# Optimization experiments

Measured on AMD Instinct MI355X. Metric: run time of the kernel, lower is better.

Reference implementation:

```python
import jax, jax.numpy as jnp
import numpy as np

B, T, D, H, K = 2, 1024, 1024, 16, 64
DMIX, DDEC, DA = 32, 64, 64
EPS = 1e-5 * 64  # GroupNorm eps = 1e-5 * head_size_divisor**2


def setup_inputs() -> dict:
    keys = jax.random.split(jax.random.key(0), 12)
    r01 = 12.0 / 23.0   # layer_id / (num_hidden_layers - 1)
    r1a0 = 0.5          # 1 - layer_id / num_hidden_layers
    ddd = np.arange(D, dtype=np.float32) / D
    maa = lambda p: jnp.asarray((1.0 - ddd ** p).reshape(1, 1, D), jnp.float32)
    decay = -6.0 + 5.0 * (np.arange(D, dtype=np.float32) / (D - 1)) ** (0.7 + 1.3 * r01)
    u = lambda i, s: jax.random.uniform(keys[i], s, jnp.float32, -0.01, 0.01)
    lin = lambda i: jax.random.normal(keys[i], (D, D), jnp.float32) / np.sqrt(D)
    return dict(
        x=jax.random.normal(keys[0], (B, T, D), jnp.float32),
        time_maa_x=maa(r1a0), time_maa_w=maa(r1a0), time_maa_k=maa(r1a0),
        time_maa_v=jnp.asarray((1.0 - (ddd ** r1a0 + 0.3 * r01)).reshape(1, 1, D), jnp.float32),
        time_maa_r=maa(0.5 * r1a0), time_maa_g=maa(0.5 * r1a0), time_maa_a=maa(r1a0),
        time_maa_w1=u(1, (D, DMIX * 6)), time_maa_w2=u(2, (6, DMIX, D)),
        time_decay=jnp.asarray(decay.reshape(1, 1, D), jnp.float32),
        time_decay_w1=u(3, (D, DDEC)), time_decay_w2=u(4, (DDEC, D)),
        a0=jnp.zeros((1, 1, D), jnp.float32),
        a1=u(5, (D, DA)) * 10.0,
        a2=jax.random.normal(keys[6], (DA, D), jnp.float32) * 0.1,
        k_k=jnp.full((1, 1, D), 0.85, jnp.float32),
        k_a=jnp.ones((1, 1, D), jnp.float32),
        W_r=lin(7), W_k=lin(8), W_v=lin(9), W_g=lin(10), W_o=lin(11),
        ln_w=jnp.ones((D,), jnp.float32), ln_b=jnp.zeros((D,), jnp.float32),
    )


def reference(x, time_maa_x, time_maa_w, time_maa_k, time_maa_v, time_maa_r,
              time_maa_g, time_maa_a, time_maa_w1, time_maa_w2, time_decay,
              time_decay_w1, time_decay_w2, a0, a1, a2, k_k, k_a,
              W_r, W_k, W_v, W_g, W_o, ln_w, ln_b):
    Bx, Tx, Dx = x.shape
    # bidirectional token shift: mean of left/right neighbors
    left = jnp.pad(x[:, :-1], ((0, 0), (1, 0), (0, 0)))
    right = jnp.pad(x[:, 1:], ((0, 0), (0, 1), (0, 0)))
    dxprev = (left + right) * 0.5 - x

    # data-dependent mixing coefficients (6-way LoRA)
    xxx = x + dxprev * time_maa_x
    hmix = jnp.tanh(xxx @ time_maa_w1).reshape(Bx, Tx, 6, DMIX)
    mix = jnp.einsum('btsm,smd->sbtd', hmix, time_maa_w2)  # (6,B,T,D)
    mw, mk, mv, mr, mg, ma = mix
    xw = x + dxprev * (time_maa_w + mw)
    xk = x + dxprev * (time_maa_k + mk)
    xv = x + dxprev * (time_maa_v + mv)
    xr = x + dxprev * (time_maa_r + mr)
    xg = x + dxprev * (time_maa_g + mg)
    xa = x + dxprev * (time_maa_a + ma)

    r = xr @ W_r
    k = xk @ W_k
    v = xv @ W_v
    g = jax.nn.silu(xg @ W_g)
    w = time_decay + jnp.tanh(xw @ time_decay_w1) @ time_decay_w2
    iclr = jax.nn.sigmoid(a0 + (xa @ a1) @ a2)
    kkh = (k * k_k).reshape(Bx, Tx, H, K)
    kk = kkh / jnp.maximum(jnp.linalg.norm(kkh, axis=-1, keepdims=True), 1e-12)
    kk = kk.reshape(Bx, Tx, Dx)
    k = k * (1.0 + (iclr - 1.0) * k_a)

    heads = lambda t: t.reshape(Bx, Tx, H, K).transpose(0, 2, 1, 3)  # (B,H,T,K)
    r_h, k_h, v_h, kk_h, iclr_h = map(heads, (r, k, v, kk, iclr))
    w_h = -jnp.exp(heads(w))

    # LION bidirectional attention with delta correction (quadratic form)
    cs = jnp.cumsum(w_h, axis=2)
    cs_b = cs - w_h
    cs_f = jnp.clip(cs - cs[:, :, Tx // 2:Tx // 2 + 1, :], -60.0, 60.0)
    cs_bs = jnp.clip(cs_b - cs_b[:, :, Tx // 2:Tx // 2 + 1, :], -60.0, 60.0)
    A_fwd = jnp.tril(jnp.einsum('bhik,bhjk->bhij', r_h * jnp.exp(cs_f), k_h * jnp.exp(-cs_f)))
    A_bwd = jnp.triu(jnp.einsum('bhik,bhjk->bhij', r_h * jnp.exp(-cs_bs), k_h * jnp.exp(cs_bs)), k=1)
    kk_corr = jnp.einsum('bhik,bhjk->bhij', kk_h * iclr_h, kk_h)
    A_df = -jnp.tril(A_fwd @ jnp.tril(kk_corr, -1))
    A_db = -jnp.triu(A_bwd @ jnp.triu(kk_corr, 1), k=1)
    y = (A_fwd + A_bwd + A_df + A_db) @ v_h  # (B,H,T,K)

    # GroupNorm(n_head groups) over flattened tokens
    y = y.transpose(0, 2, 1, 3).reshape(Bx * Tx, H, K)
    mu = y.mean(axis=-1, keepdims=True)
    var = y.var(axis=-1, keepdims=True)
    y = (y - mu) / jnp.sqrt(var + EPS)
    y = y.reshape(Bx, Tx, Dx) * ln_w + ln_b
    return (y * g) @ W_o
```

## Files before the change

### kernel.cpp

```cpp
#include <hip/hip_runtime.h>
#include <math.h>

#define BB 2
#define TT 1024
#define DD 1024
#define HH 16
#define KK 64
#define NBT 2048
#define NE  2097152ULL

typedef unsigned short u16;
typedef __attribute__((ext_vector_type(8))) short short8;
typedef __attribute__((ext_vector_type(4))) short short4v;
typedef __attribute__((ext_vector_type(4))) float f32x4;

__device__ __forceinline__ float bf2f(u16 u) {
  union { unsigned int i; float f; } v; v.i = ((unsigned int)u) << 16; return v.f;
}
__device__ __forceinline__ u16 f2bf(float x) {
  union { float f; unsigned int u; } v; v.f = x;
  unsigned int r = v.u + 0x7fffu + ((v.u >> 16) & 1u);
  return (u16)(r >> 16);
}
__device__ __forceinline__ f32x4 MFMA(short8 a, short8 b, f32x4 c) {
  return __builtin_amdgcn_mfma_f32_16x16x32_bf16(a, b, c, 0, 0, 0);
}
__device__ __forceinline__ int swzb(int row, int kbyte) {
  return row * 128 + (kbyte ^ ((row & 7) << 4));
}
__device__ __forceinline__ void gload16(const void* g, void* l) {
  __builtin_amdgcn_global_load_lds((const __attribute__((address_space(1))) void*)g,
                                   (__attribute__((address_space(3))) void*)l, 16, 0, 0);
}

__global__ __launch_bounds__(256)
void pre(const float* __restrict__ W2, u16* __restrict__ W2t,
         const float* __restrict__ W1, u16* __restrict__ W1t,
         const float* __restrict__ wdec2, const float* __restrict__ a2,
         u16* __restrict__ wdec2t, u16* __restrict__ a2t,
         const float* __restrict__ wdec1, const float* __restrict__ a1,
         u16* __restrict__ wdec1t, u16* __restrict__ a1t,
         const float* __restrict__ x, const float* __restrict__ maa_x,
         u16* __restrict__ xxx_b) {
  __shared__ float tl[64][65];
  int idx = blockIdx.x;
  int tid = threadIdx.x;
  if (idx < 96) {
    int s = idx >> 4, d0 = (idx & 15) * 64;
    int c = tid & 63, r0 = (tid >> 6) * 8;
#pragma unroll
    for (int j = 0; j < 8; ++j)
      tl[r0 + j][c] = W2[(size_t)(s * 32 + r0 + j) * 1024 + d0 + c];
    __syncthreads();
    int d = tid >> 2, ms = (tid & 3) * 8;
    u16 o[8];
#pragma unroll
    for (int j = 0; j < 8; ++j) o[j] = f2bf(tl[ms + j][d]);
    *(short8*)(W2t + ((size_t)s * 1024 + d0 + d) * 32 + ms) = *(short8*)o;
  } else if (idx < 144) {
    int i = idx - 96;
    int k0 = (i & 15) * 64, n0 = (i >> 4) * 64;
    int r = tid >> 2, c0 = (tid & 3) * 16;
#pragma unroll
    for (int j = 0; j < 16; j += 4) {
      f32x4 v = *(const f32x4*)(W1 + (size_t)(k0 + r) * 192 + n0 + c0 + j);
      tl[r][c0 + j + 0] = v[0]; tl[r][c0 + j + 1] = v[1];
      tl[r][c0 + j + 2] = v[2]; tl[r][c0 + j + 3] = v[3];
    }
    __syncthreads();
    u16 o[16];
#pragma unroll
    for (int j = 0; j < 16; ++j) o[j] = f2bf(tl[c0 + j][r]);
    *(short8*)(W1t + (size_t)(n0 + r) * 1024 + k0 + c0) = *(short8*)(o);
    *(short8*)(W1t + (size_t)(n0 + r) * 1024 + k0 + c0 + 8) = *(short8*)(o + 8);
  } else if (idx < 176) {
    int i = idx - 144;
    int zz = i >> 4;
    const float* W = zz ? a2 : wdec2;
    u16* Wt = zz ? a2t : wdec2t;
    int n0 = (i & 15) * 64;
    int r = tid >> 2, c0 = (tid & 3) * 16;
#pragma unroll
    for (int j = 0; j < 16; j += 4) {
      f32x4 v = *(const f32x4*)(W + (size_t)r * 1024 + n0 + c0 + j);
      tl[r][c0 + j + 0] = v[0]; tl[r][c0 + j + 1] = v[1];
      tl[r][c0 + j + 2] = v[2]; tl[r][c0 + j + 3] = v[3];
    }
    __syncthreads();
    u16 o[16];
#pragma unroll
    for (int j = 0; j < 16; ++j) o[j] = f2bf(tl[c0 + j][r]);
    *(short8*)(Wt + (size_t)(n0 + r) * 64 + c0) = *(short8*)(o);
    *(short8*)(Wt + (size_t)(n0 + r) * 64 + c0 + 8) = *(short8*)(o + 8);
  } else if (idx < 208) {
    int i = idx - 176;
    int zz = i >> 4;
    const float* W = zz ? a1 : wdec1;
    u16* Wt = zz ? a1t : wdec1t;
    int k0 = (i & 15) * 64;
    int r = tid >> 2, c0 = (tid & 3) * 16;
#pragma unroll
    for (int j = 0; j < 16; j += 4) {
      f32x4 v = *(const f32x4*)(W + (size_t)(k0 + r) * 64 + c0 + j);
      tl[r][c0 + j + 0] = v[0]; tl[r][c0 + j + 1] = v[1];
      tl[r][c0 + j + 2] = v[2]; tl[r][c0 + j + 3] = v[3];
    }
    __syncthreads();
    u16 o[16];
#pragma unroll
    for (int j = 0; j < 16; ++j) o[j] = f2bf(tl[c0 + j][r]);
    *(short8*)(Wt + (size_t)r * 1024 + k0 + c0) = *(short8*)(o);
    *(short8*)(Wt + (size_t)r * 1024 + k0 + c0 + 8) = *(short8*)(o + 8);
  } else {
    int row = idx - 208;
    int t = row & (TT - 1);
    int d0 = tid * 4;
    size_t g = (size_t)row * DD + d0;
    f32x4 xc = *(const f32x4*)(x + g);
    f32x4 xl = {0.f, 0.f, 0.f, 0.f}, xr = {0.f, 0.f, 0.f, 0.f};
    if (t != 0) xl = *(const f32x4*)(x + g - DD);
    if (t != TT - 1) xr = *(const f32x4*)(x + g + DD);
    f32x4 mx = *(const f32x4*)(maa_x + d0);
    u16 o[4];
#pragma unroll
    for (int j = 0; j < 4; ++j)
      o[j] = f2bf(xc[j] + (0.5f * (xl[j] + xr[j]) - xc[j]) * mx[j]);
    *(short4v*)(xxx_b + g) = *(short4v*)o;
  }
}

__global__ __launch_bounds__(256)
void hmix_g(const float* __restrict__ W_r, const float* __restrict__ W_k,
            const float* __restrict__ W_v, const float* __restrict__ W_g,
            const float* __restrict__ W_o,
            u16* __restrict__ TR, u16* __restrict__ TK, u16* __restrict__ TV,
            u16* __restrict__ TG, u16* __restrict__ TO,
            const u16* __restrict__ xxx_b, const u16* __restrict__ W1t,
            float* __restrict__ P3) {
  __shared__ float tl[64][65];
  __shared__ u16 As[4096];
  __shared__ u16 Bs[2048];
  int idx = blockIdx.x;
  int tid = threadIdx.x;
  if (idx < 1280) {
    int z = idx >> 8, rem = idx & 255;
    const float* W = (z == 0) ? W_r : (z == 1) ? W_k : (z == 2) ? W_v : (z == 3) ? W_g : W_o;
    u16* Wt = (z == 0) ? TR : (z == 1) ? TK : (z == 2) ? TV : (z == 3) ? TG : TO;
    int k0 = (rem & 15) * 64, n0 = (rem >> 4) * 64;
    int r = tid >> 2, c0 = (tid & 3) * 16;
#pragma unroll
    for (int j = 0; j < 16; j += 4) {
      f32x4 v = *(const f32x4*)(W + (size_t)(k0 + r) * 1024 + n0 + c0 + j);
      tl[r][c0 + j + 0] = v[0]; tl[r][c0 + j + 1] = v[1];
      tl[r][c0 + j + 2] = v[2]; tl[r][c0 + j + 3] = v[3];
    }
    __syncthreads();
    u16 o[16];
#pragma unroll
    for (int j = 0; j < 16; ++j) o[j] = f2bf(tl[c0 + j][r]);
    *(short8*)(Wt + (size_t)(n0 + r) * 1024 + k0 + c0) = *(short8*)(o);
    *(short8*)(Wt + (size_t)(n0 + r) * 1024 + k0 + c0 + 8) = *(short8*)(o + 8);
    return;
  }
  int i = idx - 1280;
  int n0 = (i % 3) * 64;
  int q = i / 3;
  int m0 = (q & 15) * 128;
  int kb = q >> 4;
  int w = tid >> 6, lane = tid & 63;
  int mq = w >> 1, nq = w & 1;
  f32x4 acc[4][2];
#pragma unroll
  for (int ii = 0; ii < 4; ++ii)
#pragma unroll
    for (int j = 0; j < 2; ++j) acc[ii][j] = {0.f, 0.f, 0.f, 0.f};
  for (int t = 0; t < 4; ++t) {
    int k0 = kb * 128 + t * 32;
#pragma unroll
    for (int c2 = 0; c2 < 2; ++c2) {
      int ch = w * 2 + c2;
      int row = ch * 16 + (lane >> 2);
      gload16(xxx_b + (size_t)(m0 + row) * 1024 + k0 + (lane & 3) * 8, As + ch * 512);
    }
    {
      int row = w * 16 + (lane >> 2);
      gload16(W1t + (size_t)(n0 + row) * 1024 + k0 + (lane & 3) * 8, Bs + w * 512);
    }
    __syncthreads();
    short8 a[4], b[2];
#pragma unroll
    for (int mf = 0; mf < 4; ++mf)
      a[mf] = *(const short8*)(As + (mq * 64 + mf * 16 + (lane & 15)) * 32 + (lane >> 4) * 8);
#pragma unroll
    for (int nf = 0; nf < 2; ++nf)
      b[nf] = *(const short8*)(Bs + (nq * 32 + nf * 16 + (lane & 15)) * 32 + (lane >> 4) * 8);
#pragma unroll
    for (int mf = 0; mf < 4; ++mf)
#pragma unroll
      for (int nf = 0; nf < 2; ++nf) acc[mf][nf] = MFMA(a[mf], b[nf], acc[mf][nf]);
    __syncthreads();
  }
#pragma unroll
  for (int mf = 0; mf < 4; ++mf) {
#pragma unroll
    for (int nf = 0; nf < 2; ++nf) {
      int mb = m0 + mq * 64 + mf * 16 + (lane >> 4) * 4;
      int n = n0 + nq * 32 + nf * 16 + (lane & 15);
#pragma unroll
      for (int r = 0; r < 4; ++r)
        P3[(size_t)kb * 393216 + (size_t)(mb + r) * 192 + n] = acc[mf][nf][r];
    }
  }
}

__global__ __launch_bounds__(256)
void reduce8b(const float* __restrict__ P, u16* __restrict__ C, int total) {
  size_t i = (size_t)blockIdx.x * 256 + threadIdx.x;
  float s = 0.f;
#pragma unroll
  for (int kb = 0; kb < 8; ++kb) s += P[(size_t)kb * total + i];
  C[i] = f2bf(tanhf(s));
}

__global__ __launch_bounds__(256)
void reduce8_pairb(const float* __restrict__ Pw, const float* __restrict__ Pa,
                   u16* __restrict__ hdec_b, u16* __restrict__ ha_b) {
  int z = blockIdx.y;
  size_t i = (size_t)blockIdx.x * 256 + threadIdx.x;
  const float* P = z ? Pa : Pw;
  float s = 0.f;
#pragma unroll
  for (int kb = 0; kb < 8; ++kb) s += P[(size_t)kb * 131072 + i];
  if (z) ha_b[i] = f2bf(s);
  else hdec_b[i] = f2bf(tanhf(s));
}

__global__ __launch_bounds__(256)
void mixg(const u16* __restrict__ hmixb, const u16* __restrict__ W2t,
          const float* __restrict__ x,
          const float* __restrict__ maa_w, const float* __restrict__ maa_k,
          const float* __restrict__ maa_v, const float* __restrict__ maa_r,
          const float* __restrict__ maa_g, const float* __restrict__ maa_a,
          u16* __restrict__ xw_b, u16* __restrict__ xa_b,
          u16* __restrict__ xk_b, u16* __restrict__ xv_b,
          u16* __restrict__ xr_b, u16* __restrict__ xg_b) {
  __shared__ u16 shm[16384];
  u16* As = shm;
  u16* Bs = shm + 4096;
  u16* mixt = shm;
  int s = blockIdx.z;
  int m0 = blockIdx.y * 128, n0 = blockIdx.x * 128;
  int tid = threadIdx.x, w = tid >> 6, lane = tid & 63;
  int mq = w >> 1, nq = w & 1;
#pragma unroll
  for (int c2 = 0; c2 < 2; ++c2) {
    int ch = w * 2 + c2;
    int row = ch * 16 + (lane >> 2);
    gload16(hmixb + (size_t)(m0 + row) * 192 + s * 32 + (lane & 3) * 8, As + ch * 512);
    gload16(W2t + ((size_t)s * 1024 + n0 + row) * 32 + (lane & 3) * 8, Bs + ch * 512);
  }
  __syncthreads();
  short8 a[4], b[4];
#pragma unroll
  for (int mf = 0; mf < 4; ++mf)
    a[mf] = *(const short8*)(As + (mq * 64 + mf * 16 + (lane & 15)) * 32 + (lane >> 4) * 8);
#pragma unroll
  for (int nf = 0; nf < 4; ++nf)
    b[nf] = *(const short8*)(Bs + (nq * 64 + nf * 16 + (lane & 15)) * 32 + (lane >> 4) * 8);
  f32x4 acc[4][4];
#pragma unroll
  for (int mf = 0; mf < 4; ++mf)
#pragma unroll
    for (int nf = 0; nf < 4; ++nf) {
      f32x4 z = {0.f, 0.f, 0.f, 0.f};
      acc[mf][nf] = MFMA(a[mf], b[nf], z);
    }
  __syncthreads();
#pragma unroll
  for (int mf = 0; mf < 4; ++mf) {
#pragma unroll
    for (int nf = 0; nf < 4; ++nf) {
      int col = nq * 64 + nf * 16 + (lane & 15);
#pragma unroll
      for (int r = 0; r < 4; ++r) {
        int row = mq * 64 + mf * 16 + (lane >> 4) * 4 + r;
        mixt[row * 128 + col] = f2bf(acc[mf][nf][r]);
      }
    }
  }
  __syncthreads();
  const float* maa = (s == 0) ? maa_w : (s == 1) ? maa_k : (s == 2) ? maa_v
                    : (s == 3) ? maa_r : (s == 4) ? maa_g : maa_a;
  u16* dst = (s == 0) ? xw_b : (s == 1) ? xk_b : (s == 2) ? xv_b
            : (s == 3) ? xr_b : (s == 4) ? xg_b : xa_b;
  int cg = tid & 15;
  int rowg = tid >> 4;
  int d0 = n0 + cg * 8;
  f32x4 ma0 = *(const f32x4*)(maa + d0);
  f32x4 ma1 = *(const f32x4*)(maa + d0 + 4);
#pragma unroll
  for (int rr = 0; rr < 8; ++rr) {
    int row = rr * 16 + rowg;
    int m = m0 + row;
    int t = m & (TT - 1);
    size_t g = (size_t)m * DD + d0;
    f32x4 xc0 = *(const f32x4*)(x + g);
    f32x4 xc1 = *(const f32x4*)(x + g + 4);
    f32x4 xl0 = {0.f, 0.f, 0.f, 0.f}, xl1 = {0.f, 0.f, 0.f, 0.f};
    f32x4 xr0 = {0.f, 0.f, 0.f, 0.f}, xr1 = {0.f, 0.f, 0.f, 0.f};
    if (t != 0) { xl0 = *(const f32x4*)(x + g - DD); xl1 = *(const f32x4*)(x + g - DD + 4); }
    if (t != TT - 1) { xr0 = *(const f32x4*)(x + g + DD); xr1 = *(const f32x4*)(x + g + DD + 4); }
    short8 mv = *(const short8*)(mixt + row * 128 + cg * 8);
    u16 o[8];
#pragma unroll
    for (int j = 0; j < 8; ++j) {
      float xcj = (j < 4) ? xc0[j & 3] : xc1[j & 3];
      float xlj = (j < 4) ? xl0[j & 3] : xl1[j & 3];
      float xrj = (j < 4) ? xr0[j & 3] : xr1[j & 3];
      float maj = (j < 4) ? ma0[j & 3] : ma1[j & 3];
      float dx = 0.5f * (xlj + xrj) - xcj;
      o[j] = f2bf(xcj + dx * (maj + bf2f((u16)mv[j])));
    }
    *(short8*)(dst + g) = *(short8*)o;
  }
}

__global__ __launch_bounds__(256)
void gemm_bf4(const u16* __restrict__ xr, const u16* __restrict__ xk,
              const u16* __restrict__ xv, const u16* __restrict__ xg,
              const u16* __restrict__ WtR, const u16* __restrict__ WtK,
              const u16* __restrict__ WtV, const u16* __restrict__ WtG,
              u16* __restrict__ rbuf, u16* __restrict__ kbuf,
              u16* __restrict__ vT, u16* __restrict__ gb,
              const u16* __restrict__ xw_b, const u16* __restrict__ wdec1t,
              float* __restrict__ PpartW,
              const u16* __restrict__ xa_b, const u16* __restrict__ a1t,
              float* __restrict__ PpartA) {
  __shared__ u16 As[2][4096];
  __shared__ u16 Bs[2][2048];
  int wgid = blockIdx.x;
  int tid = threadIdx.x, w = tid >> 6, lane = tid & 63;
  int mq = w >> 1, nq = w & 1;
  if (wgid >= 1024) {
    int i = wgid - 1024;
    int m0 = (i & 15) * 128;
    int kb = (i >> 4) & 7;
    int z = i >> 7;
    const u16* A = z ? xa_b : xw_b;
    const u16* Bt = z ? a1t : wdec1t;
    float* P = z ? PpartA : PpartW;
    f32x4 acc[4][2];
#pragma unroll
    for (int ii = 0; ii < 4; ++ii)
#pragma unroll
      for (int j = 0; j < 2; ++j) acc[ii][j] = {0.f, 0.f, 0.f, 0.f};
    for (int t = 0; t < 4; ++t) {
      int k0 = kb * 128 + t * 32;
#pragma unroll
      for (int c2 = 0; c2 < 2; ++c2) {
        int ch = w * 2 + c2;
        int row = ch * 16 + (lane >> 2);
        gload16(A + (size_t)(m0 + row) * 1024 + k0 + (lane & 3) * 8, As[0] + ch * 512);
      }
      {
        int row = w * 16 + (lane >> 2);
        gload16(Bt + (size_t)row * 1024 + k0 + (lane & 3) * 8, Bs[0] + w * 512);
      }
      __syncthreads();
      short8 a[4], b[2];
#pragma unroll
      for (int mf = 0; mf < 4; ++mf)
        a[mf] = *(const short8*)(As[0] + (mq * 64 + mf * 16 + (lane & 15)) * 32 + (lane >> 4) * 8);
#pragma unroll
      for (int nf = 0; nf < 2; ++nf)
        b[nf] = *(const short8*)(Bs[0] + (nq * 32 + nf * 16 + (lane & 15)) * 32 + (lane >> 4) * 8);
#pragma unroll
      for (int mf = 0; mf < 4; ++mf)
#pragma unroll
        for (int nf = 0; nf < 2; ++nf) acc[mf][nf] = MFMA(a[mf], b[nf], acc[mf][nf]);
      __syncthreads();
    }
#pragma unroll
    for (int mf = 0; mf < 4; ++mf) {
#pragma unroll
      for (int nf = 0; nf < 2; ++nf) {
        int mb = m0 + mq * 64 + mf * 16 + (lane >> 4) * 4;
        int n = nq * 32 + nf * 16 + (lane & 15);
#pragma unroll
        for (int r = 0; r < 4; ++r)
          P[(size_t)kb * 131072 + (size_t)(mb + r) * 64 + n] = acc[mf][nf][r];
      }
    }
    return;
  }
  int xcd = wgid & 7, idx = wgid >> 3;
  int z = xcd >> 1, mhalf = xcd & 1;
  int mloc = idx & 7, nt = idx >> 3;
  int m0 = (mhalf * 8 + mloc) * 128;
  int n0 = nt * 64;
  const u16* A = (z == 0) ? xr : (z == 1) ? xk : (z == 2) ? xv : xg;
  const u16* Bt = (z == 0) ? WtR : (z == 1) ? WtK : (z == 2) ? WtV : WtG;
  int arow0 = (w * 2) * 16 + (lane >> 2);
  int arow1 = (w * 2 + 1) * 16 + (lane >> 2);
  int brow = w * 16 + (lane >> 2);
  int kc = (lane & 3) * 8;
  f32x4 acc[4][2];
#pragma unroll
  for (int i = 0; i < 4; ++i)
#pragma unroll
    for (int j = 0; j < 2; ++j) acc[i][j] = {0.f, 0.f, 0.f, 0.f};
  gload16(A + (size_t)(m0 + arow0) * 1024 + kc, As[0] + (w * 2) * 512);
  gload16(A + (size_t)(m0 + arow1) * 1024 + kc, As[0] + (w * 2 + 1) * 512);
  gload16(Bt + (size_t)(n0 + brow) * 1024 + kc, Bs[0] + w * 512);
  __syncthreads();
  for (int t = 0; t < 32; ++t) {
    int cur = t & 1;
    if (t < 31) {
      int kn = (t + 1) * 32;
      gload16(A + (size_t)(m0 + arow0) * 1024 + kn + kc, As[cur ^ 1] + (w * 2) * 512);
      gload16(A + (size_t)(m0 + arow1) * 1024 + kn + kc, As[cur ^ 1] + (w * 2 + 1) * 512);
      gload16(Bt + (size_t)(n0 + brow) * 1024 + kn + kc, Bs[cur ^ 1] + w * 512);
    }
    short8 a[4], b[2];
#pragma unroll
    for (int mf = 0; mf < 4; ++mf)
      a[mf] = *(const short8*)(As[cur] + (mq * 64 + mf * 16 + (lane & 15)) * 32 + (lane >> 4) * 8);
#pragma unroll
    for (int nf = 0; nf < 2; ++nf)
      b[nf] = *(const short8*)(Bs[cur] + (nq * 32 + nf * 16 + (lane & 15)) * 32 + (lane >> 4) * 8);
#pragma unroll
    for (int mf = 0; mf < 4; ++mf)
#pragma unroll
      for (int nf = 0; nf < 2; ++nf) acc[mf][nf] = MFMA(a[mf], b[nf], acc[mf][nf]);
    __syncthreads();
  }
#pragma unroll
  for (int mf = 0; mf < 4; ++mf) {
#pragma unroll
    for (int nf = 0; nf < 2; ++nf) {
      int mb = m0 + mq * 64 + mf * 16 + (lane >> 4) * 4;
      int n = n0 + nq * 32 + nf * 16 + (lane & 15);
      if (z == 2) {
        u16 o[4];
#pragma unroll
        for (int r = 0; r < 4; ++r) o[r] = f2bf(acc[mf][nf][r]);
        int b2 = mb >> 10, t = mb & 1023;
        *(short4v*)(vT + (((size_t)(b2 * HH + (n >> 6))) * KK + (n & 63)) * TT + t) = *(short4v*)o;
      } else if (z == 3) {
#pragma unroll
        for (int r = 0; r < 4; ++r) {
          int m = mb + r;
          float v = acc[mf][nf][r];
          gb[(size_t)m * 1024 + n] = f2bf(v / (1.f + __expf(-v)));
        }
      } else {
        u16* C = (z == 0) ? rbuf : kbuf;
#pragma unroll
        for (int r = 0; r < 4; ++r) {
          int m = mb + r;
          int b2 = m >> 10, t = m & 1023;
          C[(((size_t)(b2 * HH + (n >> 6))) * TT + t) * KK + (n & 63)] = f2bf(acc[mf][nf][r]);
        }
      }
    }
  }
}

__global__ __launch_bounds__(256)
void gemm_bfo(const u16* __restrict__ A, const u16* __restrict__ Bt,
              float* __restrict__ C) {
  __shared__ u16 As[2][4096];
  __shared__ u16 Bs[2][2048];
  int wgid = blockIdx.x;
  int xcd = wgid & 7, idx = wgid >> 3;
  int mloc = idx & 1, nt = idx >> 1;
  int m0 = (xcd * 2 + mloc) * 128;
  int n0 = nt * 64;
  int tid = threadIdx.x, w = tid >> 6, lane = tid & 63;
  int mq = w >> 1, nq = w & 1;
  int arow0 = (w * 2) * 16 + (lane >> 2);
  int arow1 = (w * 2 + 1) * 16 + (lane >> 2);
  int brow = w * 16 + (lane >> 2);
  int kc = (lane & 3) * 8;
  f32x4 acc[4][2];
#pragma unroll
  for (int i = 0; i < 4; ++i)
#pragma unroll
    for (int j = 0; j < 2; ++j) acc[i][j] = {0.f, 0.f, 0.f, 0.f};
  gload16(A + (size_t)(m0 + arow0) * 1024 + kc, As[0] + (w * 2) * 512);
  gload16(A + (size_t)(m0 + arow1) * 1024 + kc, As[0] + (w * 2 + 1) * 512);
  gload16(Bt + (size_t)(n0 + brow) * 1024 + kc, Bs[0] + w * 512);
  __syncthreads();
  for (int t = 0; t < 32; ++t) {
    int cur = t & 1;
    if (t < 31) {
      int kn = (t + 1) * 32;
      gload16(A + (size_t)(m0 + arow0) * 1024 + kn + kc, As[cur ^ 1] + (w * 2) * 512);
      gload16(A + (size_t)(m0 + arow1) * 1024 + kn + kc, As[cur ^ 1] + (w * 2 + 1) * 512);
      gload16(Bt + (size_t)(n0 + brow) * 1024 + kn + kc, Bs[cur ^ 1] + w * 512);
    }
    short8 a[4], b[2];
#pragma unroll
    for (int mf = 0; mf < 4; ++mf)
      a[mf] = *(const short8*)(As[cur] + (mq * 64 + mf * 16 + (lane & 15)) * 32 + (lane >> 4) * 8);
#pragma unroll
    for (int nf = 0; nf < 2; ++nf)
      b[nf] = *(const short8*)(Bs[cur] + (nq * 32 + nf * 16 + (lane & 15)) * 32 + (lane >> 4) * 8);
#pragma unroll
    for (int mf = 0; mf < 4; ++mf)
#pragma unroll
      for (int nf = 0; nf < 2; ++nf) acc[mf][nf] = MFMA(a[mf], b[nf], acc[mf][nf]);
    __syncthreads();
  }
#pragma unroll
  for (int mf = 0; mf < 4; ++mf) {
#pragma unroll
    for (int nf = 0; nf < 2; ++nf) {
      int mb = m0 + mq * 64 + mf * 16 + (lane >> 4) * 4;
      int n = n0 + nq * 32 + nf * 16 + (lane & 15);
#pragma unroll
      for (int r = 0; r < 4; ++r)
        C[(size_t)(mb + r) * 1024 + n] = acc[mf][nf][r];
    }
  }
}

__global__ __launch_bounds__(256)
void gemm_k2b(const u16* __restrict__ A0, const u16* __restrict__ B0t,
              float* __restrict__ C0, const float* __restrict__ bias0,
              const u16* __restrict__ A1, const u16* __restrict__ B1t,
              float* __restrict__ C1, const float* __restrict__ bias1) {
  __shared__ u16 As[8192];
  __shared__ u16 Bs[4096];
  int z = blockIdx.z;
  const u16* A = z ? A1 : A0;
  const u16* Bt = z ? B1t : B0t;
  float* C = z ? C1 : C0;
  const float* bias = z ? bias1 : bias0;
  int n0 = blockIdx.x * 64, m0 = blockIdx.y * 128;
  int tid = threadIdx.x, w = tid >> 6, lane = tid & 63;
  int mq = w >> 1, nq = w & 1;
#pragma unroll
  for (int j = 0; j < 4; ++j) {
    int q = w * 4 + j;
    int ks = q >> 3, rg = q & 7;
    int row = rg * 16 + (lane >> 2);
    int kc = ks * 32 + (lane & 3) * 8;
    gload16(A + (size_t)(m0 + row) * 64 + kc, As + q * 512);
  }
#pragma unroll
  for (int j = 0; j < 2; ++j) {
    int q = w * 2 + j;
    int ks = q >> 2, rg = q & 3;
    int row = rg * 16 + (lane >> 2);
    int kc = ks * 32 + (lane & 3) * 8;
    gload16(Bt + (size_t)(n0 + row) * 64 + kc, Bs + q * 512);
  }
  __syncthreads();
  f32x4 acc[4][2];
#pragma unroll
  for (int i = 0; i < 4; ++i)
#pragma unroll
    for (int j = 0; j < 2; ++j) acc[i][j] = {0.f, 0.f, 0.f, 0.f};
#pragma unroll
  for (int ks = 0; ks < 2; ++ks) {
    short8 a[4], b[2];
#pragma unroll
    for (int mf = 0; mf < 4; ++mf)
      a[mf] = *(const short8*)(As + ks * 4096 + (mq * 64 + mf * 16 + (lane & 15)) * 32 + (lane >> 4) * 8);
#pragma unroll
    for (int nf = 0; nf < 2; ++nf)
      b[nf] = *(const short8*)(Bs + ks * 2048 + (nq * 32 + nf * 16 + (lane & 15)) * 32 + (lane >> 4) * 8);
#pragma unroll
    for (int mf = 0; mf < 4; ++mf)
#pragma unroll
      for (int nf = 0; nf < 2; ++nf) acc[mf][nf] = MFMA(a[mf], b[nf], acc[mf][nf]);
  }
#pragma unroll
  for (int mf = 0; mf < 4; ++mf) {
#pragma unroll
    for (int nf = 0; nf < 2; ++nf) {
      int mb = m0 + mq * 64 + mf * 16 + (lane >> 4) * 4;
      int n = n0 + nq * 32 + nf * 16 + (lane & 15);
      float bv = bias[n];
#pragma unroll
      for (int r = 0; r < 4; ++r) {
        int m = mb + r;
        int b2 = m >> 10, t = m & 1023;
        float vv = acc[mf][nf][r] + bv;
        if (z) vv = 1.f / (1.f + expf(-vv));
        C[(((size_t)(b2 * HH + (n >> 6))) * TT + t) * KK + (n & 63)] = vv;
      }
    }
  }
}

__global__ __launch_bounds__(256)
void k4k5(u16* __restrict__ kbuf, u16* __restrict__ kkbuf, u16* __restrict__ kkibuf,
          const float* __restrict__ iclr, const float* __restrict__ k_k,
          const float* __restrict__ k_a,
          const float* __restrict__ csf, float* __restrict__ csbs,
          float* __restrict__ part) {
  int idx = blockIdx.x;
  int tid = threadIdx.x;
  if (idx < 8192) {
    int gid = idx * 4 + (tid >> 6);
    int lane = tid & 63;
    size_t base = (size_t)gid * 64 + lane;
    int h = (gid >> 10) & (HH - 1);
    int d = h * 64 + lane;
    float kv = bf2f(kbuf[base]);
    float ic = iclr[base];
    float kkh = kv * k_k[d];
    float ss = kkh * kkh;
#pragma unroll
    for (int off = 32; off > 0; off >>= 1) ss += __shfl_xor(ss, off);
    float nrm = fmaxf(sqrtf(ss), 1e-12f);
    float kkv = kkh / nrm;
    kkbuf[base] = f2bf(kkv);
    kkibuf[base] = f2bf(kkv * ic);
    kbuf[base] = f2bf(kv * (1.f + (ic - 1.f) * k_a[d]));
  } else {
    int bc = (idx - 8192) * 4 + (tid >> 6);
    int bh = bc >> 4, c = bc & 15;
    int lane = tid & 63;
    size_t base = (size_t)bh * TT * KK + (size_t)c * 64 * KK + lane;
    float p = 0.f;
    for (int i = 0; i < 64; ++i) {
      float wh = -expf(csf[base + (size_t)i * KK]);
      csbs[base + (size_t)i * KK] = wh;
      p += wh;
    }
    part[((size_t)bh * 16 + c) * 64 + lane] = p;
  }
}

struct SReg { short8 a0, a1, b0, b1; };
template <int RSA, int RSB>
__device__ __forceinline__ void sload(const u16* ka, const u16* vb, SReg& r) {
  int t0 = threadIdx.x, t1 = threadIdx.x + 256;
  r.a0 = *(const short8*)(ka + (size_t)(t0 >> 3) * RSA + (t0 & 7) * 8);
  r.a1 = *(const short8*)(ka + (size_t)(t1 >> 3) * RSA + (t1 & 7) * 8);
  r.b0 = *(const short8*)(vb + (size_t)(t0 >> 3) * RSB + (t0 & 7) * 8);
  r.b1 = *(const short8*)(vb + (size_t)(t1 >> 3) * RSB + (t1 & 7) * 8);
}
__device__ __forceinline__ void swrite(u16* Kt, u16* Vt, const SReg& r) {
  int t0 = threadIdx.x, t1 = threadIdx.x + 256;
  *(short8*)((char*)Kt + swzb(t0 >> 3, (t0 & 7) * 16)) = r.a0;
  *(short8*)((char*)Kt + swzb(t1 >> 3, (t1 & 7) * 16)) = r.a1;
  *(short8*)((char*)Vt + swzb(t0 >> 3, (t0 & 7) * 16)) = r.b0;
  *(short8*)((char*)Vt + swzb(t1 >> 3, (t1 & 7) * 16)) = r.b1;
}
template <int MASK>
__device__ __forceinline__ void store_S(const f32x4 s[4], u16* St, int lane, int w) {
  int ig0 = w * 16 + (lane >> 4) * 4;
#pragma unroll
  for (int jf = 0; jf < 4; ++jf) {
    int jl = jf * 16 + (lane & 15);
#pragma unroll
    for (int r = 0; r < 4; ++r) {
      int il = ig0 + r;
      float v = s[jf][r];
      if (MASK == 1 && !(jl < il)) v = 0.f;
      if (MASK == 2 && !(jl > il)) v = 0.f;
      if (MASK == 3 && !(jl <= il)) v = 0.f;
      *(u16*)((char*)St + swzb(il, jl * 2)) = f2bf(v);
    }
  }
}
__device__ __forceinline__ void smm(short8 a0, short8 a1, const u16* Kt, f32x4 s[4], int lane) {
  __builtin_amdgcn_s_setprio(1);
#pragma unroll
  for (int jf = 0; jf < 4; ++jf) {
    f32x4 z = {0.f, 0.f, 0.f, 0.f};
    short8 kb0 = *(const short8*)((const char*)Kt + swzb(jf * 16 + (lane & 15), (lane >> 4) * 16));
    z = MFMA(a0, kb0, z);
    short8 kb1 = *(const short8*)((const char*)Kt + swzb(jf * 16 + (lane & 15), 64 + (lane >> 4) * 16));
    z = MFMA(a1, kb1, z);
    s[jf] = z;
  }
  __builtin_amdgcn_s_setprio(0);
}
__device__ __forceinline__ void pv(const u16* St, const u16* Vt, f32x4 acc[4], int lane, int w) {
  __builtin_amdgcn_s_setprio(1);
#pragma unroll
  for (int ks = 0; ks < 2; ++ks) {
    short8 a = *(const short8*)((const char*)St + swzb(w * 16 + (lane & 15), ks * 64 + (lane >> 4) * 16));
#pragma unroll
    for (int cf = 0; cf < 4; ++cf) {
      short8 b = *(const short8*)((const char*)Vt + swzb(cf * 16 + (lane & 15), ks * 64 + (lane >> 4) * 16));
      acc[cf] = MFMA(a, b, acc[cf]);
    }
  }
  __builtin_amdgcn_s_setprio(0);
}

__global__ __launch_bounds__(256)
void k6_pass1(const u16* __restrict__ kk, const u16* __restrict__ kki,
              const u16* __restrict__ vT, u16* __restrict__ vfT, u16* __restrict__ vbT,
              const float* __restrict__ csbs, const float* __restrict__ part,
              const u16* __restrict__ rb, const u16* __restrict__ kb,
              u16* __restrict__ rfb, u16* __restrict__ rbb,
              u16* __restrict__ kfb, u16* __restrict__ kbw) {
  __shared__ u16 Kt[2][4096], Vt[2][4096], St[4096];
  int wg = blockIdx.x;
  int tid = threadIdx.x;
  if (wg >= 1024) {
    int bc = (wg - 1024) * 4 + (tid >> 6);
    int bh = bc >> 4, c = bc & 15;
    int lane = tid & 63;
    size_t hb = (size_t)bh * TT * KK;
    float run = 0.f, csb512 = 0.f;
    for (int cc = 0; cc < 16; ++cc) {
      float pvv = part[((size_t)bh * 16 + cc) * 64 + lane];
      if (cc < c) run += pvv;
      if (cc < 8) csb512 += pvv;
    }
    float wh512 = csbs[hb + (size_t)512 * KK + lane];
    float cs512 = csb512 + wh512;
    size_t base = hb + (size_t)c * 64 * KK + lane;
    float cs = run;
    for (int i = 0; i < 64; ++i) {
      size_t g = base + (size_t)i * KK;
      float wh = csbs[g];
      cs += wh;
      float cf = fminf(fmaxf(cs - cs512, -60.f), 60.f);
      float cb = fminf(fmaxf((cs - wh) - csb512, -60.f), 60.f);
      float rvf = bf2f(rb[g]);
      float kvf = bf2f(kb[g]);
      rfb[g] = f2bf(rvf * __expf(cf));
      kfb[g] = f2bf(kvf * __expf(-cf));
      rbb[g] = f2bf(rvf * __expf(-cb));
      kbw[g] = f2bf(kvf * __expf(cb));
    }
    return;
  }
  int dir = (wg >= 512);
  int w0 = dir ? wg - 512 : wg;
  int bh = w0 & 31, it = w0 >> 5, i0 = it * 64;
  size_t hb = (size_t)bh * 65536;
  int w = tid >> 6, lane = tid & 63;
  int iw = i0 + w * 16;
  int row = iw + (lane & 15), ko = (lane >> 4) * 8;
  short8 a0 = *(const short8*)(kki + hb + (size_t)row * 64 + ko);
  short8 a1 = *(const short8*)(kki + hb + (size_t)row * 64 + 32 + ko);
  f32x4 acc[4];
#pragma unroll
  for (int c = 0; c < 4; ++c) acc[c] = {0.f, 0.f, 0.f, 0.f};
  int s0 = dir ? it : 0;
  int nph = dir ? 16 - it : it + 1;
  SReg sr, nx;
  sload<64, 1024>(kk + hb + (size_t)s0 * 4096, vT + hb + s0 * 64, sr);
  swrite(Kt[0], Vt[0], sr);
  __syncthreads();
  for (int p = 0; p < nph; ++p) {
    int s = s0 + p;
    int cur = p & 1;
    if (p < nph - 1)
      sload<64, 1024>(kk + hb + (size_t)(s + 1) * 4096, vT + hb + (s + 1) * 64, nx);
    f32x4 sv[4];
    smm(a0, a1, Kt[cur], sv, lane);
    if (s == it) {
      if (dir) store_S<2>(sv, St, lane, w);
      else store_S<1>(sv, St, lane, w);
    } else {
      store_S<0>(sv, St, lane, w);
    }
    pv(St, Vt[cur], acc, lane, w);
    if (p < nph - 1) swrite(Kt[cur ^ 1], Vt[cur ^ 1], nx);
    __syncthreads();
  }
  u16* dst = dir ? vbT : vfT;
#pragma unroll
  for (int cf = 0; cf < 4; ++cf) {
    int c = cf * 16 + (lane & 15);
    int i = iw + (lane >> 4) * 4;
    size_t g = hb + (size_t)c * 1024 + i;
    short4v vv = *(const short4v*)(vT + g);
    u16 o1[4];
#pragma unroll
    for (int r = 0; r < 4; ++r)
      o1[r] = f2bf(bf2f((u16)vv[r]) - acc[cf][r]);
    *(short4v*)(dst + g) = *(short4v*)o1;
  }
}

__global__ __launch_bounds__(256)
void k7_pass2(const u16* __restrict__ rfb, const u16* __restrict__ rbb,
              const u16* __restrict__ kfb, const u16* __restrict__ kbw,
              const u16* __restrict__ vfT, const u16* __restrict__ vbT,
              float* __restrict__ yf, float* __restrict__ yb) {
  __shared__ u16 Kt[2][4096], Vt[2][4096], St[4096];
  int wg = blockIdx.x;
  int dir = (wg >= 512);
  int w0 = dir ? wg - 512 : wg;
  int bh = w0 & 31, it = w0 >> 5, i0 = it * 64;
  size_t hb = (size_t)bh * 65536;
  int tid = threadIdx.x, w = tid >> 6, lane = tid & 63;
  int iw = i0 + w * 16;
  int row = iw + (lane & 15), ko = (lane >> 4) * 8;
  const u16* rp = dir ? rbb : rfb;
  const u16* kp = dir ? kbw : kfb;
  const u16* vp = dir ? vbT : vfT;
  short8 a0 = *(const short8*)(rp + hb + (size_t)row * 64 + ko);
  short8 a1 = *(const short8*)(rp + hb + (size_t)row * 64 + 32 + ko);
  f32x4 acc[4];
#pragma unroll
  for (int c = 0; c < 4; ++c) acc[c] = {0.f, 0.f, 0.f, 0.f};
  int s0 = dir ? it : 0;
  int nph = dir ? 16 - it : it + 1;
  SReg sr, nx;
  sload<64, 1024>(kp + hb + (size_t)s0 * 4096, vp + hb + s0 * 64, sr);
  swrite(Kt[0], Vt[0], sr);
  __syncthreads();
  for (int p = 0; p < nph; ++p) {
    int s = s0 + p;
    int cur = p & 1;
    if (p < nph - 1)
      sload<64, 1024>(kp + hb + (size_t)(s + 1) * 4096, vp + hb + (s + 1) * 64, nx);
    f32x4 sv[4];
    smm(a0, a1, Kt[cur], sv, lane);
    if (s == it) {
      if (dir) store_S<2>(sv, St, lane, w);
      else store_S<3>(sv, St, lane, w);
    } else {
      store_S<0>(sv, St, lane, w);
    }
    pv(St, Vt[cur], acc, lane, w);
    if (p < nph - 1) swrite(Kt[cur ^ 1], Vt[cur ^ 1], nx);
    __syncthreads();
  }
  float* y = dir ? yb : yf;
#pragma unroll
  for (int cf = 0; cf < 4; ++cf) {
    int c = cf * 16 + (lane & 15);
#pragma unroll
    for (int r = 0; r < 4; ++r) {
      int i = iw + (lane >> 4) * 4 + r;
      y[hb + (size_t)i * 64 + c] = acc[cf][r];
    }
  }
}

__global__ __launch_bounds__(256)
void k8_gn2(const float* __restrict__ yf, const float* __restrict__ yb,
            const u16* __restrict__ g, const float* __restrict__ lnw,
            const float* __restrict__ lnb, u16* __restrict__ outb) {
  int bt = blockIdx.x;
  int b = bt >> 10, t = bt & 1023;
  int wv = threadIdx.x >> 6, lane = threadIdx.x & 63;
  for (int h = wv; h < HH; h += 4) {
    size_t idx = (((size_t)(b * HH + h)) * TT + t) * KK + lane;
    float v = yf[idx] + yb[idx];
    float s1 = v, s2 = v * v;
#pragma unroll
    for (int off = 32; off > 0; off >>= 1) {
      s1 += __shfl_xor(s1, off);
      s2 += __shfl_xor(s2, off);
    }
    float mu = s1 * (1.f / 64.f);
    float var = s2 * (1.f / 64.f) - mu * mu;
    float xn = (v - mu) * rsqrtf(var + 6.4e-4f);
    int d = h * 64 + lane;
    float o = xn * lnw[d] + lnb[d];
    outb[(size_t)bt * DD + d] = f2bf(o * bf2f(g[(size_t)bt * DD + d]));
  }
}

extern "C" void kernel_launch(void* const* d_in, const int* in_sizes, int n_in,
                              void* d_out, int out_size, void* d_ws, size_t ws_size,
                              hipStream_t stream) {
  const float* x      = (const float*)d_in[0];
  const float* maa_x  = (const float*)d_in[1];
  const float* maa_w  = (const float*)d_in[2];
  const float* maa_k  = (const float*)d_in[3];
  const float* maa_v  = (const float*)d_in[4];
  const float* maa_r  = (const float*)d_in[5];
  const float* maa_g  = (const float*)d_in[6];
  const float* maa_a  = (const float*)d_in[7];
  const float* w1mix  = (const float*)d_in[8];
  const float* w2mix  = (const float*)d_in[9];
  const float* tdecay = (const float*)d_in[10];
  const float* wdec1  = (const float*)d_in[11];
  const float* wdec2  = (const float*)d_in[12];
  const float* a0     = (const float*)d_in[13];
  const float* a1     = (const float*)d_in[14];
  const float* a2     = (const float*)d_in[15];
  const float* k_k    = (const float*)d_in[16];
  const float* k_a    = (const float*)d_in[17];
  const float* W_r    = (const float*)d_in[18];
  const float* W_k    = (const float*)d_in[19];
  const float* W_v    = (const float*)d_in[20];
  const float* W_g    = (const float*)d_in[21];
  const float* W_o    = (const float*)d_in[22];
  const float* lnw    = (const float*)d_in[23];
  const float* lnb    = (const float*)d_in[24];
  float* out = (float*)d_out;

  const size_t NEf = NE;
  float* F = (float*)d_ws;
  u16*   xxx_b  = (u16*)F;
  u16*   xw_b   = (u16*)(F + 1 * NEf);
  u16*   xa_b   = (u16*)(F + 2 * NEf);
  float* csfb   = F + 3 * NEf;
  float* csbsb  = F + 4 * NEf;
  float* P3     = F + 3 * NEf;
  float* PpartW = F + 3 * NEf;
  float* PpartA = F + 4 * NEf;
  float* yf     = F + 3 * NEf;
  float* yb     = F + 4 * NEf;
  float* iclr   = F + 5 * NEf;
  u16*   gb     = (u16*)(F + 6 * NEf);
  u16*   hmixb  = (u16*)(F + 7 * NEf);
  u16*   hdec_b = (u16*)(F + 7 * NEf + 524288);
  u16*   ha_b   = (u16*)(F + 7 * NEf + 786432);
  float* partb  = F + 7 * NEf + 917504;
  u16*   W1t    = (u16*)(F + 7 * NEf + 1048576);
  u16*   wdec2t = (u16*)(F + 7 * NEf + 1146880);
  u16*   a2t    = (u16*)(F + 7 * NEf + 1179648);
  u16*   wdec1t = (u16*)(F + 7 * NEf + 1212416);
  u16*   a1t    = (u16*)(F + 7 * NEf + 1245184);
  u16*   W2t    = (u16*)(F + 7 * NEf + 1966080);
  u16* rfb = (u16*)xw_b;
  u16* rbb = rfb + NEf;
  u16* kfb = (u16*)xa_b;
  u16* kbw = kfb + NEf;
  u16* U = (u16*)(F + 8 * NEf);
  u16* xr_b = U + 0 * NEf;
  u16* xk_b = U + 1 * NEf;
  u16* xv_b = U + 2 * NEf;
  u16* xg_b = U + 3 * NEf;
  u16* rbuf = U + 4 * NEf;
  u16* kbuf = U + 5 * NEf;
  u16* vT   = U + 6 * NEf;
  u16* kkb  = U + 7 * NEf;
  u16* kkib = U + 8 * NEf;
  u16* vfT  = U + 9 * NEf;
  u16* vbT  = U + 10 * NEf;
  u16* gnb  = U + 11 * NEf;
  u16* WtR  = U + 12 * NEf;
  u16* WtK  = U + 12 * NEf + 1048576;
  u16* WtV  = U + 12 * NEf + 2097152;
  u16* WtG  = U + 12 * NEf + 3145728;
  u16* WtO  = U + 12 * NEf + 4194304;

  dim3 blk(256);

  pre<<<2256, blk, 0, stream>>>(w2mix, W2t, w1mix, W1t, wdec2, a2, wdec2t, a2t,
                                wdec1, a1, wdec1t, a1t, x, maa_x, xxx_b);

  hmix_g<<<1664, blk, 0, stream>>>(W_r, W_k, W_v, W_g, W_o,
                                   WtR, WtK, WtV, WtG, WtO,
                                   xxx_b, W1t, P3);
  reduce8b<<<1536, blk, 0, stream>>>(P3, hmixb, 393216);

  mixg<<<dim3(8, 16, 6), blk, 0, stream>>>(hmixb, W2t, x,
                                           maa_w, maa_k, maa_v, maa_r, maa_g, maa_a,
                                           xw_b, xa_b, xk_b, xv_b, xr_b, xg_b);

  gemm_bf4<<<1280, blk, 0, stream>>>(xr_b, xk_b, xv_b, xg_b,
                                     WtR, WtK, WtV, WtG,
                                     rbuf, kbuf, vT, gb,
                                     xw_b, wdec1t, PpartW, xa_b, a1t, PpartA);

  reduce8_pairb<<<dim3(512, 2), blk, 0, stream>>>(PpartW, PpartA, hdec_b, ha_b);
  gemm_k2b<<<dim3(16, 16, 2), blk, 0, stream>>>(hdec_b, wdec2t, csfb, tdecay,
                                                ha_b, a2t, iclr, a0);

  k4k5<<<8320, blk, 0, stream>>>(kbuf, kkb, kkib, iclr, k_k, k_a,
                                 csfb, csbsb, partb);

  k6_pass1<<<1152, blk, 0, stream>>>(kkb, kkib, vT, vfT, vbT,
                                     csbsb, partb, rbuf, kbuf,
                                     rfb, rbb, kfb, kbw);
  k7_pass2<<<1024, blk, 0, stream>>>(rfb, rbb, kfb, kbw, vfT, vbT, yf, yb);
  k8_gn2<<<NBT, blk, 0, stream>>>(yf, yb, gb, lnw, lnb, gnb);
  gemm_bfo<<<256, blk, 0, stream>>>(gnb, WtO, out);
}
```

Measured before the change: 178.6 us.

## Fuse decay exp/partial sums and kk normalization into the k2 GEMM epilogue

```diff
diff --git a/kernel.cpp b/kernel.cpp
--- a/kernel.cpp
+++ b/kernel.cpp
@@ -527,15 +527,18 @@
 
 __global__ __launch_bounds__(256)
 void gemm_k2b(const u16* __restrict__ A0, const u16* __restrict__ B0t,
-              float* __restrict__ C0, const float* __restrict__ bias0,
+              const float* __restrict__ bias0,
+              float* __restrict__ csbs, float* __restrict__ part,
               const u16* __restrict__ A1, const u16* __restrict__ B1t,
-              float* __restrict__ C1, const float* __restrict__ bias1) {
+              const float* __restrict__ bias1,
+              u16* __restrict__ kbuf, u16* __restrict__ kkb, u16* __restrict__ kkib,
+              const float* __restrict__ k_k, const float* __restrict__ k_a) {
   __shared__ u16 As[8192];
   __shared__ u16 Bs[4096];
+  __shared__ float hsum[128][2];
   int z = blockIdx.z;
   const u16* A = z ? A1 : A0;
   const u16* Bt = z ? B1t : B0t;
-  float* C = z ? C1 : C0;
   const float* bias = z ? bias1 : bias0;
   int n0 = blockIdx.x * 64, m0 = blockIdx.y * 128;
   int tid = threadIdx.x, w = tid >> 6, lane = tid & 63;
@@ -576,62 +579,102 @@
 #pragma unroll
       for (int nf = 0; nf < 2; ++nf) acc[mf][nf] = MFMA(a[mf], b[nf], acc[mf][nf]);
   }
-#pragma unroll
-  for (int mf = 0; mf < 4; ++mf) {
+  int b2 = m0 >> 10, h = n0 >> 6;
+  int bh = b2 * HH + h;
+  int jj = lane & 15, g = lane >> 4;
+  if (z == 0) {
+    float psum[2] = {0.f, 0.f};
+#pragma unroll
+    for (int mf = 0; mf < 4; ++mf) {
+      int mb = m0 + mq * 64 + mf * 16 + g * 4;
+#pragma unroll
+      for (int nf = 0; nf < 2; ++nf) {
+        int n = n0 + nq * 32 + nf * 16 + jj;
+        float bv = bias[n];
+#pragma unroll
+        for (int r = 0; r < 4; ++r) {
+          int t = (mb + r) & 1023;
+          float wh = -expf(acc[mf][nf][r] + bv);
+          csbs[(((size_t)bh) * TT + t) * KK + (n & 63)] = wh;
+          psum[nf] += wh;
+        }
+      }
+    }
 #pragma unroll
     for (int nf = 0; nf < 2; ++nf) {
-      int mb = m0 + mq * 64 + mf * 16 + (lane >> 4) * 4;
-      int n = n0 + nq * 32 + nf * 16 + (lane & 15);
-      float bv = bias[n];
+      psum[nf] += __shfl_xor(psum[nf], 16);
+      psum[nf] += __shfl_xor(psum[nf], 32);
+    }
+    if (lane < 16) {
+      int c = ((m0 & 1023) >> 6) + mq;
+#pragma unroll
+      for (int nf = 0; nf < 2; ++nf)
+        part[((size_t)bh * 16 + c) * 64 + nq * 32 + nf * 16 + jj] = psum[nf];
+    }
+  } else {
+    float kk2[2], ka2[2], icv[4][2][4], kvf[4][2][4];
+#pragma unroll
+    for (int nf = 0; nf < 2; ++nf) {
+      int n = n0 + nq * 32 + nf * 16 + jj;
+      kk2[nf] = k_k[n];
+      ka2[nf] = k_a[n];
+    }
+#pragma unroll
+    for (int mf = 0; mf < 4; ++mf) {
+      int mb = m0 + mq * 64 + mf * 16 + g * 4;
+#pragma unroll
+      for (int nf = 0; nf < 2; ++nf) {
+        int n = n0 + nq * 32 + nf * 16 + jj;
+        float bv = bias[n];
+#pragma unroll
+        for (int r = 0; r < 4; ++r) {
+          int t = (mb + r) & 1023;
+          size_t gidx = (((size_t)bh) * TT + t) * KK + (n & 63);
+          icv[mf][nf][r] = 1.f / (1.f + expf(-(acc[mf][nf][r] + bv)));
+          kvf[mf][nf][r] = bf2f(kbuf[gidx]);
+        }
+      }
+    }
+#pragma unroll
+    for (int mf = 0; mf < 4; ++mf) {
 #pragma unroll
       for (int r = 0; r < 4; ++r) {
-        int m = mb + r;
-        int b2 = m >> 10, t = m & 1023;
-        float vv = acc[mf][nf][r] + bv;
-        if (z) vv = 1.f / (1.f + expf(-vv));
-        C[(((size_t)(b2 * HH + (n >> 6))) * TT + t) * KK + (n & 63)] = vv;
+        float s = 0.f;
+#pragma unroll
+        for (int nf = 0; nf < 2; ++nf) {
+          float kkh = kvf[mf][nf][r] * kk2[nf];
+          s += kkh * kkh;
+        }
+        s += __shfl_xor(s, 1);
+        s += __shfl_xor(s, 2);
+        s += __shfl_xor(s, 4);
+        s += __shfl_xor(s, 8);
+        if (jj == 0) hsum[mq * 64 + mf * 16 + g * 4 + r][nq] = s;
       }
     }
-  }
-}
-
-__global__ __launch_bounds__(256)
-void k4k5(u16* __restrict__ kbuf, u16* __restrict__ kkbuf, u16* __restrict__ kkibuf,
-          const float* __restrict__ iclr, const float* __restrict__ k_k,
-          const float* __restrict__ k_a,
-          const float* __restrict__ csf, float* __restrict__ csbs,
-          float* __restrict__ part) {
-  int idx = blockIdx.x;
-  int tid = threadIdx.x;
-  if (idx < 8192) {
-    int gid = idx * 4 + (tid >> 6);
-    int lane = tid & 63;
-    size_t base = (size_t)gid * 64 + lane;
-    int h = (gid >> 10) & (HH - 1);
-    int d = h * 64 + lane;
-    float kv = bf2f(kbuf[base]);
-    float ic = iclr[base];
-    float kkh = kv * k_k[d];
-    float ss = kkh * kkh;
-#pragma unroll
-    for (int off = 32; off > 0; off >>= 1) ss += __shfl_xor(ss, off);
-    float nrm = fmaxf(sqrtf(ss), 1e-12f);
-    float kkv = kkh / nrm;
-    kkbuf[base] = f2bf(kkv);
-    kkibuf[base] = f2bf(kkv * ic);
-    kbuf[base] = f2bf(kv * (1.f + (ic - 1.f) * k_a[d]));
-  } else {
-    int bc = (idx - 8192) * 4 + (tid >> 6);
-    int bh = bc >> 4, c = bc & 15;
-    int lane = tid & 63;
-    size_t base = (size_t)bh * TT * KK + (size_t)c * 64 * KK + lane;
-    float p = 0.f;
-    for (int i = 0; i < 64; ++i) {
-      float wh = -expf(csf[base + (size_t)i * KK]);
-      csbs[base + (size_t)i * KK] = wh;
-      p += wh;
-    }
-    part[((size_t)bh * 16 + c) * 64 + lane] = p;
+    __syncthreads();
+#pragma unroll
+    for (int mf = 0; mf < 4; ++mf) {
+      int mb = m0 + mq * 64 + mf * 16 + g * 4;
+#pragma unroll
+      for (int r = 0; r < 4; ++r) {
+        int rl = mq * 64 + mf * 16 + g * 4 + r;
+        float ss = hsum[rl][0] + hsum[rl][1];
+        float nrm = fmaxf(sqrtf(ss), 1e-12f);
+        int t = (mb + r) & 1023;
+#pragma unroll
+        for (int nf = 0; nf < 2; ++nf) {
+          int n = n0 + nq * 32 + nf * 16 + jj;
+          size_t gidx = (((size_t)bh) * TT + t) * KK + (n & 63);
+          float kkh = kvf[mf][nf][r] * kk2[nf];
+          float kkv = kkh / nrm;
+          float ic = icv[mf][nf][r];
+          kkb[gidx] = f2bf(kkv);
+          kkib[gidx] = f2bf(kkv * ic);
+          kbuf[gidx] = f2bf(kvf[mf][nf][r] * (1.f + (ic - 1.f) * ka2[nf]));
+        }
+      }
+    }
   }
 }
 
@@ -902,14 +945,12 @@
   u16*   xxx_b  = (u16*)F;
   u16*   xw_b   = (u16*)(F + 1 * NEf);
   u16*   xa_b   = (u16*)(F + 2 * NEf);
-  float* csfb   = F + 3 * NEf;
   float* csbsb  = F + 4 * NEf;
   float* P3     = F + 3 * NEf;
   float* PpartW = F + 3 * NEf;
   float* PpartA = F + 4 * NEf;
   float* yf     = F + 3 * NEf;
-  float* yb     = F + 4 * NEf;
-  float* iclr   = F + 5 * NEf;
+  float* yb     = F + 5 * NEf;
   u16*   gb     = (u16*)(F + 6 * NEf);
   u16*   hmixb  = (u16*)(F + 7 * NEf);
   u16*   hdec_b = (u16*)(F + 7 * NEf + 524288);
@@ -964,11 +1005,10 @@
                                      xw_b, wdec1t, PpartW, xa_b, a1t, PpartA);
 
   reduce8_pairb<<<dim3(512, 2), blk, 0, stream>>>(PpartW, PpartA, hdec_b, ha_b);
-  gemm_k2b<<<dim3(16, 16, 2), blk, 0, stream>>>(hdec_b, wdec2t, csfb, tdecay,
-                                                ha_b, a2t, iclr, a0);
-
-  k4k5<<<8320, blk, 0, stream>>>(kbuf, kkb, kkib, iclr, k_k, k_a,
-                                 csfb, csbsb, partb);
+
+  gemm_k2b<<<dim3(16, 16, 2), blk, 0, stream>>>(hdec_b, wdec2t, tdecay, csbsb, partb,
+                                                ha_b, a2t, a0,
+                                                kbuf, kkb, kkib, k_k, k_a);
 
   k6_pass1<<<1152, blk, 0, stream>>>(kkb, kkib, vT, vfT, vbT,
                                      csbsb, partb, rbuf, kbuf,
```

Measured after the change: 170.2 us. 1.05x faster.
